# Performance work log

Hardware: AMD Instinct MI355X
Metric: run time of the kernel (lower is better)

## Reference

```python
import jax, jax.numpy as jnp
import numpy as np

GRID = (32, 32)       # SOM grid shape
INPUT_DIM = 512
BATCH = 16384
TAU = 0.5             # softmax temperature
EPS = 1e-8


def setup_inputs() -> dict:
    key = jax.random.key(0)
    k1, k2 = jax.random.split(key)
    x = jax.random.normal(k1, (BATCH, INPUT_DIM), dtype=jnp.float32)
    # glorot_uniform for shape (*GRID, INPUT_DIM): fan_in = 32*32, fan_out = 512
    fan_in, fan_out = GRID[0] * GRID[1], INPUT_DIM
    limit = float(np.sqrt(6.0 / (fan_in + fan_out)))
    weights_map = jax.random.uniform(
        k2, (*GRID, INPUT_DIM), dtype=jnp.float32, minval=-limit, maxval=limit
    )
    return {"x": x, "weights_map": weights_map}


def reference(x, weights_map):
    """SoftSOM forward: squared distances -> per-dimension softmax -> soft reconstruction."""
    B, D = x.shape
    gh, gw = GRID
    w_flat = weights_map.reshape(gh * gw, D)  # [N, D]
    d2 = (
        jnp.sum(x * x, axis=-1, keepdims=True)           # [B,1]
        + jnp.sum(w_flat * w_flat, axis=-1)[None, :]     # [1,N]
        - 2.0 * (x @ w_flat.T)                           # [B,N]
    )
    logits = (-d2 / TAU).reshape(B, gh, gw)
    # per-dimension softmax: softmax along each grid axis, combined multiplicatively
    s_rows = jax.nn.softmax(logits, axis=1)   # softmax over grid dim 0
    s_cols = jax.nn.softmax(logits, axis=2)   # softmax over grid dim 1
    a = s_rows * s_cols
    a = a / (jnp.sum(a, axis=(1, 2), keepdims=True) + EPS)  # renormalize over grid
    # soft reconstruction: weighted sum of prototypes
    y = jnp.einsum("bij,ijd->bd", a, weights_map)  # [B, D]
    return y
```

## Files before the change

### kernel.cpp

```cpp
#include <hip/hip_runtime.h>
#include <hip/hip_bf16.h>
#include <stdint.h>

#define B_SZ 16384
#define D_SZ 512
#define N_SZ 1024

using f16x8 = __attribute__((ext_vector_type(8))) _Float16;
using f16x4 = __attribute__((ext_vector_type(4))) _Float16;
using f32x4 = __attribute__((ext_vector_type(4))) float;

typedef unsigned int u32_as1 __attribute__((address_space(1)));
typedef unsigned int u32_as3 __attribute__((address_space(3)));

__device__ __forceinline__ void gload16(const void* g, void* lds_base) {
    __builtin_amdgcn_global_load_lds((const u32_as1*)g, (u32_as3*)lds_base, 16, 0, 0);
}

__device__ __forceinline__ unsigned short f16bits(_Float16 h) {
    return __builtin_bit_cast(unsigned short, h);
}

__global__ __launch_bounds__(256) void prep(
    const float* __restrict__ W, const float* __restrict__ X,
    _Float16* __restrict__ wh, _Float16* __restrict__ wt,
    float* __restrict__ ww, _Float16* __restrict__ xh) {
    const int bid = blockIdx.x;
    const int t = threadIdx.x;
    if (bid < 32) {
        __shared__ unsigned int cells[512 * 17];
        const int n0 = bid * 32;
        const int np = t >> 4;
        const int dc = t & 15;
        const int na = n0 + 2 * np, nb = na + 1;
        const int d0 = dc * 32;
        float va[32], vb[32];
#pragma unroll
        for (int i = 0; i < 8; ++i) {
            *reinterpret_cast<float4*>(&va[i * 4]) =
                *reinterpret_cast<const float4*>(&W[(size_t)na * D_SZ + d0 + i * 4]);
            *reinterpret_cast<float4*>(&vb[i * 4]) =
                *reinterpret_cast<const float4*>(&W[(size_t)nb * D_SZ + d0 + i * 4]);
        }
        float sa = 0.f, sb = 0.f;
#pragma unroll
        for (int i = 0; i < 32; ++i) { sa += va[i] * va[i]; sb += vb[i] * vb[i]; }
        sa += __shfl_xor(sa, 1); sa += __shfl_xor(sa, 2);
        sa += __shfl_xor(sa, 4); sa += __shfl_xor(sa, 8);
        sb += __shfl_xor(sb, 1); sb += __shfl_xor(sb, 2);
        sb += __shfl_xor(sb, 4); sb += __shfl_xor(sb, 8);
        if (dc == 0) { ww[na] = sa; ww[nb] = sb; }
        _Float16 ha[32], hb[32];
#pragma unroll
        for (int i = 0; i < 32; ++i) { ha[i] = (_Float16)va[i]; hb[i] = (_Float16)vb[i]; }
        unsigned int pa[16], pb[16];
#pragma unroll
        for (int j = 0; j < 16; ++j) {
            pa[j] = (unsigned)f16bits(ha[2 * j]) | ((unsigned)f16bits(ha[2 * j + 1]) << 16);
            pb[j] = (unsigned)f16bits(hb[2 * j]) | ((unsigned)f16bits(hb[2 * j + 1]) << 16);
        }
        unsigned int* whU = reinterpret_cast<unsigned int*>(wh);
#pragma unroll
        for (int j = 0; j < 4; ++j) {
            *reinterpret_cast<uint4*>(&whU[((size_t)na * D_SZ + d0) / 2 + j * 4]) =
                make_uint4(pa[j * 4], pa[j * 4 + 1], pa[j * 4 + 2], pa[j * 4 + 3]);
            *reinterpret_cast<uint4*>(&whU[((size_t)nb * D_SZ + d0) / 2 + j * 4]) =
                make_uint4(pb[j * 4], pb[j * 4 + 1], pb[j * 4 + 2], pb[j * 4 + 3]);
        }
#pragma unroll
        for (int k = 0; k < 32; ++k) {
            const int d = d0 + k;
            const unsigned u = (unsigned)f16bits(ha[k]) | ((unsigned)f16bits(hb[k]) << 16);
            cells[d * 17 + (np ^ ((d >> 5) & 15))] = u;
        }
        __syncthreads();
        for (int rr = 0; rr < 2; ++rr) {
            const int d = 2 * t + rr;
            const int px = (d >> 5) & 15;
            unsigned int buf[16];
#pragma unroll
            for (int j = 0; j < 16; ++j) buf[j] = cells[d * 17 + (j ^ px)];
            unsigned int* wtU = reinterpret_cast<unsigned int*>(wt);
#pragma unroll
            for (int j = 0; j < 4; ++j)
                *reinterpret_cast<uint4*>(&wtU[((size_t)d * N_SZ + n0) / 2 + j * 4]) =
                    make_uint4(buf[j * 4], buf[j * 4 + 1], buf[j * 4 + 2], buf[j * 4 + 3]);
        }
    } else {
        const int b2 = bid - 32;
        const int chunk = (b2 & 7) * 512 + (b2 >> 3);
        const size_t idx = ((size_t)chunk * 256 + t) * 8;
        const float4 a = *reinterpret_cast<const float4*>(&X[idx]);
        const float4 b = *reinterpret_cast<const float4*>(&X[idx + 4]);
        f16x8 h = {(_Float16)a.x, (_Float16)a.y, (_Float16)a.z, (_Float16)a.w,
                   (_Float16)b.x, (_Float16)b.y, (_Float16)b.z, (_Float16)b.w};
        *reinterpret_cast<f16x8*>(&xh[idx]) = h;
    }
}

__global__ __launch_bounds__(256, 4) void gemm1(
    const _Float16* __restrict__ xh, const _Float16* __restrict__ wh,
    const float* __restrict__ ww, _Float16* __restrict__ L16) {
    __shared__ _Float16 smem[16384];
    const int tid = threadIdx.x;
    const int wid = tid >> 6, lane = tid & 63;
    const int raw = blockIdx.y * 8 + blockIdx.x;
    const int wsw = (raw & 7) * 128 + (raw >> 3);
    const int bn0 = (wsw & 7) * 128;
    const int bm0 = (wsw >> 3) * 128;
    const int m0 = (wid >> 1) * 64, n0 = (wid & 1) * 64;
    const int rA = lane & 15;
    const int cbr = (lane >> 4) * 16;
    const int rswz = ((rA >> 1) & 3) << 4;

    const int br0 = (wid * 2) * 16 + (lane >> 2);
    const int br1 = (wid * 2 + 1) * 16 + (lane >> 2);
    const int sg0 = ((lane & 3) ^ ((br0 >> 1) & 3)) * 8;
    const int sg1 = ((lane & 3) ^ ((br1 >> 1) & 3)) * 8;
    const int bdst0 = (wid * 2) * 1024;
    const int bdst1 = (wid * 2 + 1) * 1024;
    char* const As_b = (char*)smem;
    char* const Bs_b = (char*)smem + 16384;

    f32x4 acc[4][4];
    for (int mi = 0; mi < 4; ++mi)
        for (int ni = 0; ni < 4; ++ni) acc[mi][ni] = (f32x4){0.f, 0.f, 0.f, 0.f};

    gload16(&xh[(size_t)(bm0 + br0) * D_SZ + sg0], As_b + bdst0);
    gload16(&xh[(size_t)(bm0 + br1) * D_SZ + sg1], As_b + bdst1);
    gload16(&wh[(size_t)(bn0 + br0) * D_SZ + sg0], Bs_b + bdst0);
    gload16(&wh[(size_t)(bn0 + br1) * D_SZ + sg1], Bs_b + bdst1);
    __syncthreads();

    int cur = 0;
    for (int kt = 0; kt < 16; ++kt) {
        const int nxt = cur ^ 1;
        if (kt < 15) {
            const int gk = (kt + 1) * 32;
            gload16(&xh[(size_t)(bm0 + br0) * D_SZ + gk + sg0], As_b + nxt * 8192 + bdst0);
            gload16(&xh[(size_t)(bm0 + br1) * D_SZ + gk + sg1], As_b + nxt * 8192 + bdst1);
            gload16(&wh[(size_t)(bn0 + br0) * D_SZ + gk + sg0], Bs_b + nxt * 8192 + bdst0);
            gload16(&wh[(size_t)(bn0 + br1) * D_SZ + gk + sg1], Bs_b + nxt * 8192 + bdst1);
        }
        f16x8 af[4], bf[4];
        for (int mi = 0; mi < 4; ++mi)
            af[mi] = *reinterpret_cast<const f16x8*>(
                As_b + cur * 8192 + (m0 + mi * 16 + rA) * 64 + (cbr ^ rswz));
        for (int ni = 0; ni < 4; ++ni)
            bf[ni] = *reinterpret_cast<const f16x8*>(
                Bs_b + cur * 8192 + (n0 + ni * 16 + rA) * 64 + (cbr ^ rswz));
        for (int mi = 0; mi < 4; ++mi)
            for (int ni = 0; ni < 4; ++ni)
                acc[mi][ni] = __builtin_amdgcn_mfma_f32_16x16x32_f16(af[mi], bf[ni], acc[mi][ni], 0, 0, 0);
        __syncthreads();
        cur = nxt;
    }

    for (int mi = 0; mi < 4; ++mi)
        for (int ni = 0; ni < 4; ++ni) {
            const int ln = n0 + ni * 16 + rA;
            const float wwn = ww[bn0 + ln];
            const int lm = m0 + mi * 16 + (lane >> 4) * 4;
            const f32x4 a = acc[mi][ni];
            for (int r = 0; r < 4; ++r)
                smem[(lm + r) * 128 + ln] = (_Float16)(4.f * a[r] - 2.f * wwn);
        }
    __syncthreads();
    for (int c = 0; c < 8; ++c) {
        const int idx = c * 2048 + tid * 8;
        const int row = idx >> 7, col = idx & 127;
        const f16x8 v = *reinterpret_cast<const f16x8*>(&smem[idx]);
        *reinterpret_cast<f16x8*>(&L16[(size_t)(bm0 + row) * N_SZ + bn0 + col]) = v;
    }
}

__global__ __launch_bounds__(512) void softsm(_Float16* __restrict__ L16) {
    __shared__ float4 spart[2][4][8];
    __shared__ float mpart[2][4];
    __shared__ float Tp[2][4];
    const int h = threadIdx.x >> 8;
    const int t = threadIdx.x & 255;
    const int w = t >> 6, lane = t & 63;
    const int g8 = t & 7;
    const int bid = blockIdx.x;
    const size_t row = (size_t)(bid & 7) * 2048 + (size_t)(bid >> 3) * 2 + h;
    const f16x4 lv = *reinterpret_cast<const f16x4*>(&L16[row * N_SZ + (size_t)t * 4]);
    const float v0 = (float)lv[0], v1 = (float)lv[1], v2 = (float)lv[2], v3 = (float)lv[3];

    float m = fmaxf(fmaxf(v0, v1), fmaxf(v2, v3));
    for (int o = 32; o; o >>= 1) m = fmaxf(m, __shfl_xor(m, o));
    if (lane == 0) mpart[h][w] = m;
    __syncthreads();
    m = fmaxf(fmaxf(mpart[h][0], mpart[h][1]), fmaxf(mpart[h][2], mpart[h][3]));

    const float u0 = __expf(v0 - m), u1 = __expf(v1 - m);
    const float u2 = __expf(v2 - m), u3 = __expf(v3 - m);
    float rs = (u0 + u1) + (u2 + u3);
    rs += __shfl_xor(rs, 1); rs += __shfl_xor(rs, 2); rs += __shfl_xor(rs, 4);
    float s0 = u0, s1 = u1, s2 = u2, s3 = u3;
    for (int o = 8; o <= 32; o <<= 1) {
        s0 += __shfl_xor(s0, o); s1 += __shfl_xor(s1, o);
        s2 += __shfl_xor(s2, o); s3 += __shfl_xor(s3, o);
    }
    if (lane < 8) spart[h][w][lane] = make_float4(s0, s1, s2, s3);
    __syncthreads();
    {
        const float4 q0 = spart[h][0][g8], q1 = spart[h][1][g8];
        const float4 q2 = spart[h][2][g8], q3 = spart[h][3][g8];
        s0 = (q0.x + q1.x) + (q2.x + q3.x);
        s1 = (q0.y + q1.y) + (q2.y + q3.y);
        s2 = (q0.z + q1.z) + (q2.z + q3.z);
        s3 = (q0.w + q1.w) + (q2.w + q3.w);
    }
    const float irs = __builtin_amdgcn_rcpf(rs);
    const float t0 = u0 * u0 * irs * __builtin_amdgcn_rcpf(s0);
    const float t1 = u1 * u1 * irs * __builtin_amdgcn_rcpf(s1);
    const float t2 = u2 * u2 * irs * __builtin_amdgcn_rcpf(s2);
    const float t3 = u3 * u3 * irs * __builtin_amdgcn_rcpf(s3);
    float sT = (t0 + t1) + (t2 + t3);
    for (int o = 1; o <= 32; o <<= 1) sT += __shfl_xor(sT, o);
    if (lane == 0) Tp[h][w] = sT;
    __syncthreads();
    const float T = (Tp[h][0] + Tp[h][1]) + (Tp[h][2] + Tp[h][3]);
    const float inv = __builtin_amdgcn_rcpf(T + 1e-8f);
    f16x4 o16 = {(_Float16)(t0 * inv), (_Float16)(t1 * inv),
                 (_Float16)(t2 * inv), (_Float16)(t3 * inv)};
    *reinterpret_cast<f16x4*>(&L16[row * N_SZ + (size_t)t * 4]) = o16;
}

__global__ __launch_bounds__(256, 4) void gemm2(
    const _Float16* __restrict__ a16, const _Float16* __restrict__ wt,
    float* __restrict__ Y) {
    __shared__ _Float16 As[2 * 128 * 32];
    __shared__ _Float16 Bs[2 * 128 * 32];
    const int tid = threadIdx.x;
    const int wid = tid >> 6, lane = tid & 63;
    const int raw = blockIdx.y * 4 + blockIdx.x;
    const int wsw = (raw & 7) * 64 + (raw >> 3);
    const int bn0 = (wsw & 3) * 128;
    const int bm0 = (wsw >> 2) * 128;
    const int m0 = (wid >> 1) * 64, n0 = (wid & 1) * 64;
    const int rA = lane & 15;
    const int cbr = (lane >> 4) * 16;
    const int rswz = ((rA >> 1) & 3) << 4;

    const int br0 = (wid * 2) * 16 + (lane >> 2);
    const int br1 = (wid * 2 + 1) * 16 + (lane >> 2);
    const int sg0 = ((lane & 3) ^ ((br0 >> 1) & 3)) * 8;
    const int sg1 = ((lane & 3) ^ ((br1 >> 1) & 3)) * 8;
    const int bdst0 = (wid * 2) * 1024;
    const int bdst1 = (wid * 2 + 1) * 1024;
    char* const As_b = (char*)As;
    char* const Bs_b = (char*)Bs;

    f32x4 acc[4][4];
    for (int mi = 0; mi < 4; ++mi)
        for (int ni = 0; ni < 4; ++ni) acc[mi][ni] = (f32x4){0.f, 0.f, 0.f, 0.f};

    gload16(&a16[(size_t)(bm0 + br0) * N_SZ + sg0], As_b + bdst0);
    gload16(&a16[(size_t)(bm0 + br1) * N_SZ + sg1], As_b + bdst1);
    gload16(&wt[(size_t)(bn0 + br0) * N_SZ + sg0], Bs_b + bdst0);
    gload16(&wt[(size_t)(bn0 + br1) * N_SZ + sg1], Bs_b + bdst1);
    __syncthreads();

    int cur = 0;
    for (int kt = 0; kt < 32; ++kt) {
        const int nxt = cur ^ 1;
        if (kt < 31) {
            const int gk = (kt + 1) * 32;
            gload16(&a16[(size_t)(bm0 + br0) * N_SZ + gk + sg0], As_b + nxt * 8192 + bdst0);
            gload16(&a16[(size_t)(bm0 + br1) * N_SZ + gk + sg1], As_b + nxt * 8192 + bdst1);
            gload16(&wt[(size_t)(bn0 + br0) * N_SZ + gk + sg0], Bs_b + nxt * 8192 + bdst0);
            gload16(&wt[(size_t)(bn0 + br1) * N_SZ + gk + sg1], Bs_b + nxt * 8192 + bdst1);
        }
        f16x8 af[4], bf[4];
        for (int mi = 0; mi < 4; ++mi)
            af[mi] = *reinterpret_cast<const f16x8*>(
                As_b + cur * 8192 + (m0 + mi * 16 + rA) * 64 + (cbr ^ rswz));
        for (int ni = 0; ni < 4; ++ni)
            bf[ni] = *reinterpret_cast<const f16x8*>(
                Bs_b + cur * 8192 + (n0 + ni * 16 + rA) * 64 + (cbr ^ rswz));
        for (int mi = 0; mi < 4; ++mi)
            for (int ni = 0; ni < 4; ++ni)
                acc[mi][ni] = __builtin_amdgcn_mfma_f32_16x16x32_f16(af[mi], bf[ni], acc[mi][ni], 0, 0, 0);
        __syncthreads();
        cur = nxt;
    }
    for (int mi = 0; mi < 4; ++mi)
        for (int ni = 0; ni < 4; ++ni) {
            const int dd = bn0 + n0 + ni * 16 + rA;
            const int bb = bm0 + m0 + mi * 16 + (lane >> 4) * 4;
            const f32x4 a = acc[mi][ni];
            for (int r = 0; r < 4; ++r)
                Y[(size_t)(bb + r) * D_SZ + dd] = a[r];
        }
}

extern "C" void kernel_launch(void* const* d_in, const int* in_sizes, int n_in,
                              void* d_out, int out_size, void* d_ws, size_t ws_size,
                              hipStream_t stream) {
    (void)in_sizes; (void)n_in; (void)out_size; (void)ws_size;
    const float* X = (const float*)d_in[0];
    const float* W = (const float*)d_in[1];
    float* Y = (float*)d_out;
    char* ws = (char*)d_ws;

    _Float16* L16 = (_Float16*)ws;
    _Float16* wh  = (_Float16*)(ws + (size_t)32 * 1024 * 1024);
    _Float16* wt  = (_Float16*)(ws + (size_t)33 * 1024 * 1024);
    float*    ww  = (float*)   (ws + (size_t)34 * 1024 * 1024);
    _Float16* xh  = (_Float16*)(ws + (size_t)34 * 1024 * 1024 + 4096);

    prep<<<32 + 4096, 256, 0, stream>>>(W, X, wh, wt, ww, xh);
    gemm1<<<dim3(N_SZ / 128, B_SZ / 128), 256, 0, stream>>>(xh, wh, ww, L16);
    softsm<<<B_SZ / 2, 512, 0, stream>>>(L16);
    gemm2<<<dim3(D_SZ / 128, B_SZ / 128), 256, 0, stream>>>(L16, wt, Y);
}
```

Before: 99.46 us.

## Fuse distance GEMM, dual softmax and reconstruction GEMM into one kernel

Replaces the three kernels (gemm1, softsm, gemm2) with one fused kernel. Each 512-thread block owns 64 batch rows across all 1024 grid cells. It keeps logits in registers, does the row, column and total softmax reductions through shuffles and LDS, and writes the normalized weights to a swizzled f16 LDS tile. That tile feeds the second GEMM directly. This removes the 32 MB f16 logits buffer and its write, read and rewrite round trips through global memory. In exchange, operands are read straight from global/L2 with no LDS staging or double buffering, and the large LDS footprint allows only one block (8 waves) per CU, which risks exposed load latency.

After: 112.8 us. 13.5% more time.

```diff
diff --git a/kernel.cpp b/kernel.cpp
--- a/kernel.cpp
+++ b/kernel.cpp
@@ -7,15 +7,7 @@
 #define N_SZ 1024
 
 using f16x8 = __attribute__((ext_vector_type(8))) _Float16;
-using f16x4 = __attribute__((ext_vector_type(4))) _Float16;
 using f32x4 = __attribute__((ext_vector_type(4))) float;
-
-typedef unsigned int u32_as1 __attribute__((address_space(1)));
-typedef unsigned int u32_as3 __attribute__((address_space(3)));
-
-__device__ __forceinline__ void gload16(const void* g, void* lds_base) {
-    __builtin_amdgcn_global_load_lds((const u32_as1*)g, (u32_as3*)lds_base, 16, 0, 0);
-}
 
 __device__ __forceinline__ unsigned short f16bits(_Float16 h) {
     return __builtin_bit_cast(unsigned short, h);
@@ -98,201 +90,193 @@
     }
 }
 
-__global__ __launch_bounds__(256, 4) void gemm1(
+__global__ __launch_bounds__(512, 2) void fused(
     const _Float16* __restrict__ xh, const _Float16* __restrict__ wh,
-    const float* __restrict__ ww, _Float16* __restrict__ L16) {
-    __shared__ _Float16 smem[16384];
+    const _Float16* __restrict__ wt, const float* __restrict__ ww,
+    float* __restrict__ Y) {
+    __shared__ __align__(16) char lds[152064];
+    float* csw = (float*)lds;
+    float* rs  = (float*)(lds + 131072);
+    float* Mx  = (float*)(lds + 139264);
+    float* Tw  = (float*)(lds + 141312);
+    float* Mv  = (float*)(lds + 143360);
+    float* Tv  = (float*)(lds + 143616);
+    float* csf = (float*)(lds + 143872);
+
     const int tid = threadIdx.x;
-    const int wid = tid >> 6, lane = tid & 63;
-    const int raw = blockIdx.y * 8 + blockIdx.x;
-    const int wsw = (raw & 7) * 128 + (raw >> 3);
-    const int bn0 = (wsw & 7) * 128;
-    const int bm0 = (wsw >> 3) * 128;
-    const int m0 = (wid >> 1) * 64, n0 = (wid & 1) * 64;
-    const int rA = lane & 15;
-    const int cbr = (lane >> 4) * 16;
-    const int rswz = ((rA >> 1) & 3) << 4;
-
-    const int br0 = (wid * 2) * 16 + (lane >> 2);
-    const int br1 = (wid * 2 + 1) * 16 + (lane >> 2);
-    const int sg0 = ((lane & 3) ^ ((br0 >> 1) & 3)) * 8;
-    const int sg1 = ((lane & 3) ^ ((br1 >> 1) & 3)) * 8;
-    const int bdst0 = (wid * 2) * 1024;
-    const int bdst1 = (wid * 2 + 1) * 1024;
-    char* const As_b = (char*)smem;
-    char* const Bs_b = (char*)smem + 16384;
-
-    f32x4 acc[4][4];
-    for (int mi = 0; mi < 4; ++mi)
-        for (int ni = 0; ni < 4; ++ni) acc[mi][ni] = (f32x4){0.f, 0.f, 0.f, 0.f};
-
-    gload16(&xh[(size_t)(bm0 + br0) * D_SZ + sg0], As_b + bdst0);
-    gload16(&xh[(size_t)(bm0 + br1) * D_SZ + sg1], As_b + bdst1);
-    gload16(&wh[(size_t)(bn0 + br0) * D_SZ + sg0], Bs_b + bdst0);
-    gload16(&wh[(size_t)(bn0 + br1) * D_SZ + sg1], Bs_b + bdst1);
-    __syncthreads();
-
-    int cur = 0;
+    const int w = tid >> 6, l = tid & 63;
+    const int l4 = l >> 4, lm = l & 15;
+    const int raw = blockIdx.x;
+    const int bm0 = ((raw & 7) * 32 + (raw >> 3)) * 64;
+
+    f32x4 acc[4][8];
+#pragma unroll
+    for (int mi = 0; mi < 4; ++mi)
+#pragma unroll
+        for (int ni = 0; ni < 8; ++ni) acc[mi][ni] = (f32x4){0.f, 0.f, 0.f, 0.f};
+
     for (int kt = 0; kt < 16; ++kt) {
-        const int nxt = cur ^ 1;
-        if (kt < 15) {
-            const int gk = (kt + 1) * 32;
-            gload16(&xh[(size_t)(bm0 + br0) * D_SZ + gk + sg0], As_b + nxt * 8192 + bdst0);
-            gload16(&xh[(size_t)(bm0 + br1) * D_SZ + gk + sg1], As_b + nxt * 8192 + bdst1);
-            gload16(&wh[(size_t)(bn0 + br0) * D_SZ + gk + sg0], Bs_b + nxt * 8192 + bdst0);
-            gload16(&wh[(size_t)(bn0 + br1) * D_SZ + gk + sg1], Bs_b + nxt * 8192 + bdst1);
-        }
-        f16x8 af[4], bf[4];
+        const int gk = kt * 32;
+        f16x8 af[4], bf[8];
+#pragma unroll
         for (int mi = 0; mi < 4; ++mi)
             af[mi] = *reinterpret_cast<const f16x8*>(
-                As_b + cur * 8192 + (m0 + mi * 16 + rA) * 64 + (cbr ^ rswz));
-        for (int ni = 0; ni < 4; ++ni)
+                &xh[(size_t)(bm0 + mi * 16 + lm) * D_SZ + gk + l4 * 8]);
+#pragma unroll
+        for (int ni = 0; ni < 8; ++ni)
             bf[ni] = *reinterpret_cast<const f16x8*>(
-                Bs_b + cur * 8192 + (n0 + ni * 16 + rA) * 64 + (cbr ^ rswz));
+                &wh[(size_t)(w * 128 + ni * 16 + lm) * D_SZ + gk + l4 * 8]);
+#pragma unroll
         for (int mi = 0; mi < 4; ++mi)
-            for (int ni = 0; ni < 4; ++ni)
+#pragma unroll
+            for (int ni = 0; ni < 8; ++ni)
                 acc[mi][ni] = __builtin_amdgcn_mfma_f32_16x16x32_f16(af[mi], bf[ni], acc[mi][ni], 0, 0, 0);
-        __syncthreads();
-        cur = nxt;
-    }
-
-    for (int mi = 0; mi < 4; ++mi)
-        for (int ni = 0; ni < 4; ++ni) {
-            const int ln = n0 + ni * 16 + rA;
-            const float wwn = ww[bn0 + ln];
-            const int lm = m0 + mi * 16 + (lane >> 4) * 4;
-            const f32x4 a = acc[mi][ni];
+    }
+    float wwv[8];
+#pragma unroll
+    for (int ni = 0; ni < 8; ++ni) wwv[ni] = ww[w * 128 + ni * 16 + lm];
+#pragma unroll
+    for (int mi = 0; mi < 4; ++mi)
+#pragma unroll
+        for (int ni = 0; ni < 8; ++ni)
+#pragma unroll
             for (int r = 0; r < 4; ++r)
-                smem[(lm + r) * 128 + ln] = (_Float16)(4.f * a[r] - 2.f * wwn);
-        }
-    __syncthreads();
-    for (int c = 0; c < 8; ++c) {
-        const int idx = c * 2048 + tid * 8;
-        const int row = idx >> 7, col = idx & 127;
-        const f16x8 v = *reinterpret_cast<const f16x8*>(&smem[idx]);
-        *reinterpret_cast<f16x8*>(&L16[(size_t)(bm0 + row) * N_SZ + bn0 + col]) = v;
-    }
-}
-
-__global__ __launch_bounds__(512) void softsm(_Float16* __restrict__ L16) {
-    __shared__ float4 spart[2][4][8];
-    __shared__ float mpart[2][4];
-    __shared__ float Tp[2][4];
-    const int h = threadIdx.x >> 8;
-    const int t = threadIdx.x & 255;
-    const int w = t >> 6, lane = t & 63;
-    const int g8 = t & 7;
-    const int bid = blockIdx.x;
-    const size_t row = (size_t)(bid & 7) * 2048 + (size_t)(bid >> 3) * 2 + h;
-    const f16x4 lv = *reinterpret_cast<const f16x4*>(&L16[row * N_SZ + (size_t)t * 4]);
-    const float v0 = (float)lv[0], v1 = (float)lv[1], v2 = (float)lv[2], v3 = (float)lv[3];
-
-    float m = fmaxf(fmaxf(v0, v1), fmaxf(v2, v3));
-    for (int o = 32; o; o >>= 1) m = fmaxf(m, __shfl_xor(m, o));
-    if (lane == 0) mpart[h][w] = m;
-    __syncthreads();
-    m = fmaxf(fmaxf(mpart[h][0], mpart[h][1]), fmaxf(mpart[h][2], mpart[h][3]));
-
-    const float u0 = __expf(v0 - m), u1 = __expf(v1 - m);
-    const float u2 = __expf(v2 - m), u3 = __expf(v3 - m);
-    float rs = (u0 + u1) + (u2 + u3);
-    rs += __shfl_xor(rs, 1); rs += __shfl_xor(rs, 2); rs += __shfl_xor(rs, 4);
-    float s0 = u0, s1 = u1, s2 = u2, s3 = u3;
-    for (int o = 8; o <= 32; o <<= 1) {
-        s0 += __shfl_xor(s0, o); s1 += __shfl_xor(s1, o);
-        s2 += __shfl_xor(s2, o); s3 += __shfl_xor(s3, o);
-    }
-    if (lane < 8) spart[h][w][lane] = make_float4(s0, s1, s2, s3);
-    __syncthreads();
-    {
-        const float4 q0 = spart[h][0][g8], q1 = spart[h][1][g8];
-        const float4 q2 = spart[h][2][g8], q3 = spart[h][3][g8];
-        s0 = (q0.x + q1.x) + (q2.x + q3.x);
-        s1 = (q0.y + q1.y) + (q2.y + q3.y);
-        s2 = (q0.z + q1.z) + (q2.z + q3.z);
-        s3 = (q0.w + q1.w) + (q2.w + q3.w);
-    }
-    const float irs = __builtin_amdgcn_rcpf(rs);
-    const float t0 = u0 * u0 * irs * __builtin_amdgcn_rcpf(s0);
-    const float t1 = u1 * u1 * irs * __builtin_amdgcn_rcpf(s1);
-    const float t2 = u2 * u2 * irs * __builtin_amdgcn_rcpf(s2);
-    const float t3 = u3 * u3 * irs * __builtin_amdgcn_rcpf(s3);
-    float sT = (t0 + t1) + (t2 + t3);
-    for (int o = 1; o <= 32; o <<= 1) sT += __shfl_xor(sT, o);
-    if (lane == 0) Tp[h][w] = sT;
-    __syncthreads();
-    const float T = (Tp[h][0] + Tp[h][1]) + (Tp[h][2] + Tp[h][3]);
-    const float inv = __builtin_amdgcn_rcpf(T + 1e-8f);
-    f16x4 o16 = {(_Float16)(t0 * inv), (_Float16)(t1 * inv),
-                 (_Float16)(t2 * inv), (_Float16)(t3 * inv)};
-    *reinterpret_cast<f16x4*>(&L16[row * N_SZ + (size_t)t * 4]) = o16;
-}
-
-__global__ __launch_bounds__(256, 4) void gemm2(
-    const _Float16* __restrict__ a16, const _Float16* __restrict__ wt,
-    float* __restrict__ Y) {
-    __shared__ _Float16 As[2 * 128 * 32];
-    __shared__ _Float16 Bs[2 * 128 * 32];
-    const int tid = threadIdx.x;
-    const int wid = tid >> 6, lane = tid & 63;
-    const int raw = blockIdx.y * 4 + blockIdx.x;
-    const int wsw = (raw & 7) * 64 + (raw >> 3);
-    const int bn0 = (wsw & 3) * 128;
-    const int bm0 = (wsw >> 2) * 128;
-    const int m0 = (wid >> 1) * 64, n0 = (wid & 1) * 64;
-    const int rA = lane & 15;
-    const int cbr = (lane >> 4) * 16;
-    const int rswz = ((rA >> 1) & 3) << 4;
-
-    const int br0 = (wid * 2) * 16 + (lane >> 2);
-    const int br1 = (wid * 2 + 1) * 16 + (lane >> 2);
-    const int sg0 = ((lane & 3) ^ ((br0 >> 1) & 3)) * 8;
-    const int sg1 = ((lane & 3) ^ ((br1 >> 1) & 3)) * 8;
-    const int bdst0 = (wid * 2) * 1024;
-    const int bdst1 = (wid * 2 + 1) * 1024;
-    char* const As_b = (char*)As;
-    char* const Bs_b = (char*)Bs;
-
-    f32x4 acc[4][4];
-    for (int mi = 0; mi < 4; ++mi)
-        for (int ni = 0; ni < 4; ++ni) acc[mi][ni] = (f32x4){0.f, 0.f, 0.f, 0.f};
-
-    gload16(&a16[(size_t)(bm0 + br0) * N_SZ + sg0], As_b + bdst0);
-    gload16(&a16[(size_t)(bm0 + br1) * N_SZ + sg1], As_b + bdst1);
-    gload16(&wt[(size_t)(bn0 + br0) * N_SZ + sg0], Bs_b + bdst0);
-    gload16(&wt[(size_t)(bn0 + br1) * N_SZ + sg1], Bs_b + bdst1);
-    __syncthreads();
-
-    int cur = 0;
+                acc[mi][ni][r] = 4.f * acc[mi][ni][r] - 2.f * wwv[ni];
+
+#pragma unroll
+    for (int mi = 0; mi < 4; ++mi)
+#pragma unroll
+        for (int r = 0; r < 4; ++r) {
+            float m = acc[mi][0][r];
+#pragma unroll
+            for (int ni = 1; ni < 8; ++ni) m = fmaxf(m, acc[mi][ni][r]);
+            m = fmaxf(m, __shfl_xor(m, 1));
+            m = fmaxf(m, __shfl_xor(m, 2));
+            m = fmaxf(m, __shfl_xor(m, 4));
+            m = fmaxf(m, __shfl_xor(m, 8));
+            if (lm == 0) Mx[(mi * 16 + l4 * 4 + r) * 8 + w] = m;
+        }
+    __syncthreads();
+    if (tid < 64) {
+        float m = Mx[tid * 8];
+#pragma unroll
+        for (int k = 1; k < 8; ++k) m = fmaxf(m, Mx[tid * 8 + k]);
+        Mv[tid] = m;
+    }
+    __syncthreads();
+#pragma unroll
+    for (int mi = 0; mi < 4; ++mi)
+#pragma unroll
+        for (int r = 0; r < 4; ++r) {
+            const int b = mi * 16 + l4 * 4 + r;
+            const float Mb = Mv[b];
+            float u[8];
+#pragma unroll
+            for (int ni = 0; ni < 8; ++ni) {
+                u[ni] = __expf(acc[mi][ni][r] - Mb);
+                acc[mi][ni][r] = u[ni];
+            }
+#pragma unroll
+            for (int ip = 0; ip < 4; ++ip) {
+                float s = u[2 * ip] + u[2 * ip + 1];
+                s += __shfl_xor(s, 1); s += __shfl_xor(s, 2);
+                s += __shfl_xor(s, 4); s += __shfl_xor(s, 8);
+                if (lm == 0) rs[b * 32 + 4 * w + ip] = s;
+            }
+#pragma unroll
+            for (int jp = 0; jp < 2; ++jp) {
+                const float c = (u[jp] + u[2 + jp]) + (u[4 + jp] + u[6 + jp]);
+                csw[(w * 64 + b) * 32 + jp * 16 + lm] = c;
+            }
+        }
+    __syncthreads();
+    for (int c = tid; c < 2048; c += 512) {
+        float s = csw[c];
+#pragma unroll
+        for (int k = 1; k < 8; ++k) s += csw[k * 2048 + c];
+        csf[c] = s;
+    }
+    __syncthreads();
+#pragma unroll
+    for (int mi = 0; mi < 4; ++mi)
+#pragma unroll
+        for (int r = 0; r < 4; ++r) {
+            const int b = mi * 16 + l4 * 4 + r;
+            float rsv[4], csv[2];
+#pragma unroll
+            for (int ip = 0; ip < 4; ++ip) rsv[ip] = __builtin_amdgcn_rcpf(rs[b * 32 + 4 * w + ip]);
+#pragma unroll
+            for (int jp = 0; jp < 2; ++jp) csv[jp] = __builtin_amdgcn_rcpf(csf[b * 32 + jp * 16 + lm]);
+            float tsum = 0.f;
+#pragma unroll
+            for (int ni = 0; ni < 8; ++ni) {
+                const float uu = acc[mi][ni][r];
+                const float t = uu * uu * rsv[ni >> 1] * csv[ni & 1];
+                acc[mi][ni][r] = t;
+                tsum += t;
+            }
+            tsum += __shfl_xor(tsum, 1); tsum += __shfl_xor(tsum, 2);
+            tsum += __shfl_xor(tsum, 4); tsum += __shfl_xor(tsum, 8);
+            if (lm == 0) Tw[b * 8 + w] = tsum;
+        }
+    __syncthreads();
+    if (tid < 64) {
+        float s = Tw[tid * 8];
+#pragma unroll
+        for (int k = 1; k < 8; ++k) s += Tw[tid * 8 + k];
+        Tv[tid] = __builtin_amdgcn_rcpf(s + 1e-8f);
+    }
+    __syncthreads();
+#pragma unroll
+    for (int mi = 0; mi < 4; ++mi)
+#pragma unroll
+        for (int r = 0; r < 4; ++r) {
+            const int b = mi * 16 + l4 * 4 + r;
+            const float Tb = Tv[b];
+#pragma unroll
+            for (int ni = 0; ni < 8; ++ni) {
+                const int n = w * 128 + ni * 16 + lm;
+                const int off = b * 2048 + ((n * 2) ^ ((b & 7) << 4));
+                *reinterpret_cast<_Float16*>(lds + off) = (_Float16)(acc[mi][ni][r] * Tb);
+            }
+        }
+    __syncthreads();
+
+    f32x4 acc2[4][4];
+#pragma unroll
+    for (int mi = 0; mi < 4; ++mi)
+#pragma unroll
+        for (int di = 0; di < 4; ++di) acc2[mi][di] = (f32x4){0.f, 0.f, 0.f, 0.f};
+
     for (int kt = 0; kt < 32; ++kt) {
-        const int nxt = cur ^ 1;
-        if (kt < 31) {
-            const int gk = (kt + 1) * 32;
-            gload16(&a16[(size_t)(bm0 + br0) * N_SZ + gk + sg0], As_b + nxt * 8192 + bdst0);
-            gload16(&a16[(size_t)(bm0 + br1) * N_SZ + gk + sg1], As_b + nxt * 8192 + bdst1);
-            gload16(&wt[(size_t)(bn0 + br0) * N_SZ + gk + sg0], Bs_b + nxt * 8192 + bdst0);
-            gload16(&wt[(size_t)(bn0 + br1) * N_SZ + gk + sg1], Bs_b + nxt * 8192 + bdst1);
-        }
-        f16x8 af[4], bf[4];
+        f16x8 a4[4], b4[4];
+#pragma unroll
+        for (int mi = 0; mi < 4; ++mi) {
+            const int b = mi * 16 + lm;
+            const int off = b * 2048 + ((kt * 64 + l4 * 16) ^ ((b & 7) << 4));
+            a4[mi] = *reinterpret_cast<const f16x8*>(lds + off);
+        }
+#pragma unroll
+        for (int di = 0; di < 4; ++di) {
+            const int d = w * 64 + di * 16 + lm;
+            b4[di] = *reinterpret_cast<const f16x8*>(
+                &wt[(size_t)d * N_SZ + kt * 32 + l4 * 8]);
+        }
+#pragma unroll
         for (int mi = 0; mi < 4; ++mi)
-            af[mi] = *reinterpret_cast<const f16x8*>(
-                As_b + cur * 8192 + (m0 + mi * 16 + rA) * 64 + (cbr ^ rswz));
-        for (int ni = 0; ni < 4; ++ni)
-            bf[ni] = *reinterpret_cast<const f16x8*>(
-                Bs_b + cur * 8192 + (n0 + ni * 16 + rA) * 64 + (cbr ^ rswz));
-        for (int mi = 0; mi < 4; ++mi)
-            for (int ni = 0; ni < 4; ++ni)
-                acc[mi][ni] = __builtin_amdgcn_mfma_f32_16x16x32_f16(af[mi], bf[ni], acc[mi][ni], 0, 0, 0);
-        __syncthreads();
-        cur = nxt;
-    }
-    for (int mi = 0; mi < 4; ++mi)
-        for (int ni = 0; ni < 4; ++ni) {
-            const int dd = bn0 + n0 + ni * 16 + rA;
-            const int bb = bm0 + m0 + mi * 16 + (lane >> 4) * 4;
-            const f32x4 a = acc[mi][ni];
+#pragma unroll
+            for (int di = 0; di < 4; ++di)
+                acc2[mi][di] = __builtin_amdgcn_mfma_f32_16x16x32_f16(a4[mi], b4[di], acc2[mi][di], 0, 0, 0);
+    }
+#pragma unroll
+    for (int mi = 0; mi < 4; ++mi)
+#pragma unroll
+        for (int di = 0; di < 4; ++di) {
+            const int dd = w * 64 + di * 16 + lm;
+            const int bb = bm0 + mi * 16 + l4 * 4;
+#pragma unroll
             for (int r = 0; r < 4; ++r)
-                Y[(size_t)(bb + r) * D_SZ + dd] = a[r];
+                Y[(size_t)(bb + r) * D_SZ + dd] = acc2[mi][di][r];
         }
 }
 
@@ -305,14 +289,11 @@
     float* Y = (float*)d_out;
     char* ws = (char*)d_ws;
 
-    _Float16* L16 = (_Float16*)ws;
-    _Float16* wh  = (_Float16*)(ws + (size_t)32 * 1024 * 1024);
-    _Float16* wt  = (_Float16*)(ws + (size_t)33 * 1024 * 1024);
-    float*    ww  = (float*)   (ws + (size_t)34 * 1024 * 1024);
-    _Float16* xh  = (_Float16*)(ws + (size_t)34 * 1024 * 1024 + 4096);
+    _Float16* wh = (_Float16*)ws;
+    _Float16* wt = (_Float16*)(ws + (size_t)1 * 1024 * 1024);
+    float*    ww = (float*)   (ws + (size_t)2 * 1024 * 1024);
+    _Float16* xh = (_Float16*)(ws + (size_t)2 * 1024 * 1024 + 4096);
 
     prep<<<32 + 4096, 256, 0, stream>>>(W, X, wh, wt, ww, xh);
-    gemm1<<<dim3(N_SZ / 128, B_SZ / 128), 256, 0, stream>>>(xh, wh, ww, L16);
-    softsm<<<B_SZ / 2, 512, 0, stream>>>(L16);
-    gemm2<<<dim3(D_SZ / 128, B_SZ / 128), 256, 0, stream>>>(L16, wt, Y);
-}
+    fused<<<256, 512, 0, stream>>>(xh, wh, wt, ww, Y);
+}
```

## Fuse X fp16 conversion into gemm1 by staging fp32 tiles in LDS

Applied to the files above, without the earlier changes.

Removes the separate pass in prep that converts X to fp16 and writes it to workspace. gemm1 now DMAs fp32 rows of X straight into an XOR-swizzled LDS buffer and converts them to fp16 while building MFMA fragments. This avoids writing and re-reading a 16 MB fp16 copy of X. In exchange gemm1 reads twice as many A bytes per tile, uses 48 KB of LDS with occupancy lowered to 3 blocks, and adds conversion ALU work in the inner loop.

Measured after the change: 105.1 us. 5.7% more time.

```diff
diff --git a/kernel.cpp b/kernel.cpp
--- a/kernel.cpp
+++ b/kernel.cpp
@@ -22,86 +22,73 @@
 }
 
 __global__ __launch_bounds__(256) void prep(
-    const float* __restrict__ W, const float* __restrict__ X,
-    _Float16* __restrict__ wh, _Float16* __restrict__ wt,
-    float* __restrict__ ww, _Float16* __restrict__ xh) {
-    const int bid = blockIdx.x;
+    const float* __restrict__ W, _Float16* __restrict__ wh,
+    _Float16* __restrict__ wt, float* __restrict__ ww) {
+    __shared__ unsigned int cells[512 * 17];
     const int t = threadIdx.x;
-    if (bid < 32) {
-        __shared__ unsigned int cells[512 * 17];
-        const int n0 = bid * 32;
-        const int np = t >> 4;
-        const int dc = t & 15;
-        const int na = n0 + 2 * np, nb = na + 1;
-        const int d0 = dc * 32;
-        float va[32], vb[32];
-#pragma unroll
-        for (int i = 0; i < 8; ++i) {
-            *reinterpret_cast<float4*>(&va[i * 4]) =
-                *reinterpret_cast<const float4*>(&W[(size_t)na * D_SZ + d0 + i * 4]);
-            *reinterpret_cast<float4*>(&vb[i * 4]) =
-                *reinterpret_cast<const float4*>(&W[(size_t)nb * D_SZ + d0 + i * 4]);
-        }
-        float sa = 0.f, sb = 0.f;
-#pragma unroll
-        for (int i = 0; i < 32; ++i) { sa += va[i] * va[i]; sb += vb[i] * vb[i]; }
-        sa += __shfl_xor(sa, 1); sa += __shfl_xor(sa, 2);
-        sa += __shfl_xor(sa, 4); sa += __shfl_xor(sa, 8);
-        sb += __shfl_xor(sb, 1); sb += __shfl_xor(sb, 2);
-        sb += __shfl_xor(sb, 4); sb += __shfl_xor(sb, 8);
-        if (dc == 0) { ww[na] = sa; ww[nb] = sb; }
-        _Float16 ha[32], hb[32];
-#pragma unroll
-        for (int i = 0; i < 32; ++i) { ha[i] = (_Float16)va[i]; hb[i] = (_Float16)vb[i]; }
-        unsigned int pa[16], pb[16];
-#pragma unroll
-        for (int j = 0; j < 16; ++j) {
-            pa[j] = (unsigned)f16bits(ha[2 * j]) | ((unsigned)f16bits(ha[2 * j + 1]) << 16);
-            pb[j] = (unsigned)f16bits(hb[2 * j]) | ((unsigned)f16bits(hb[2 * j + 1]) << 16);
-        }
-        unsigned int* whU = reinterpret_cast<unsigned int*>(wh);
-#pragma unroll
-        for (int j = 0; j < 4; ++j) {
-            *reinterpret_cast<uint4*>(&whU[((size_t)na * D_SZ + d0) / 2 + j * 4]) =
-                make_uint4(pa[j * 4], pa[j * 4 + 1], pa[j * 4 + 2], pa[j * 4 + 3]);
-            *reinterpret_cast<uint4*>(&whU[((size_t)nb * D_SZ + d0) / 2 + j * 4]) =
-                make_uint4(pb[j * 4], pb[j * 4 + 1], pb[j * 4 + 2], pb[j * 4 + 3]);
-        }
-#pragma unroll
-        for (int k = 0; k < 32; ++k) {
-            const int d = d0 + k;
-            const unsigned u = (unsigned)f16bits(ha[k]) | ((unsigned)f16bits(hb[k]) << 16);
-            cells[d * 17 + (np ^ ((d >> 5) & 15))] = u;
-        }
-        __syncthreads();
-        for (int rr = 0; rr < 2; ++rr) {
-            const int d = 2 * t + rr;
-            const int px = (d >> 5) & 15;
-            unsigned int buf[16];
-#pragma unroll
-            for (int j = 0; j < 16; ++j) buf[j] = cells[d * 17 + (j ^ px)];
-            unsigned int* wtU = reinterpret_cast<unsigned int*>(wt);
-#pragma unroll
-            for (int j = 0; j < 4; ++j)
-                *reinterpret_cast<uint4*>(&wtU[((size_t)d * N_SZ + n0) / 2 + j * 4]) =
-                    make_uint4(buf[j * 4], buf[j * 4 + 1], buf[j * 4 + 2], buf[j * 4 + 3]);
-        }
-    } else {
-        const int b2 = bid - 32;
-        const int chunk = (b2 & 7) * 512 + (b2 >> 3);
-        const size_t idx = ((size_t)chunk * 256 + t) * 8;
-        const float4 a = *reinterpret_cast<const float4*>(&X[idx]);
-        const float4 b = *reinterpret_cast<const float4*>(&X[idx + 4]);
-        f16x8 h = {(_Float16)a.x, (_Float16)a.y, (_Float16)a.z, (_Float16)a.w,
-                   (_Float16)b.x, (_Float16)b.y, (_Float16)b.z, (_Float16)b.w};
-        *reinterpret_cast<f16x8*>(&xh[idx]) = h;
-    }
-}
-
-__global__ __launch_bounds__(256, 4) void gemm1(
-    const _Float16* __restrict__ xh, const _Float16* __restrict__ wh,
+    const int n0 = blockIdx.x * 32;
+    const int np = t >> 4;
+    const int dc = t & 15;
+    const int na = n0 + 2 * np, nb = na + 1;
+    const int d0 = dc * 32;
+    float va[32], vb[32];
+#pragma unroll
+    for (int i = 0; i < 8; ++i) {
+        *reinterpret_cast<float4*>(&va[i * 4]) =
+            *reinterpret_cast<const float4*>(&W[(size_t)na * D_SZ + d0 + i * 4]);
+        *reinterpret_cast<float4*>(&vb[i * 4]) =
+            *reinterpret_cast<const float4*>(&W[(size_t)nb * D_SZ + d0 + i * 4]);
+    }
+    float sa = 0.f, sb = 0.f;
+#pragma unroll
+    for (int i = 0; i < 32; ++i) { sa += va[i] * va[i]; sb += vb[i] * vb[i]; }
+    sa += __shfl_xor(sa, 1); sa += __shfl_xor(sa, 2);
+    sa += __shfl_xor(sa, 4); sa += __shfl_xor(sa, 8);
+    sb += __shfl_xor(sb, 1); sb += __shfl_xor(sb, 2);
+    sb += __shfl_xor(sb, 4); sb += __shfl_xor(sb, 8);
+    if (dc == 0) { ww[na] = sa; ww[nb] = sb; }
+    _Float16 ha[32], hb[32];
+#pragma unroll
+    for (int i = 0; i < 32; ++i) { ha[i] = (_Float16)va[i]; hb[i] = (_Float16)vb[i]; }
+    unsigned int pa[16], pb[16];
+#pragma unroll
+    for (int j = 0; j < 16; ++j) {
+        pa[j] = (unsigned)f16bits(ha[2 * j]) | ((unsigned)f16bits(ha[2 * j + 1]) << 16);
+        pb[j] = (unsigned)f16bits(hb[2 * j]) | ((unsigned)f16bits(hb[2 * j + 1]) << 16);
+    }
+    unsigned int* whU = reinterpret_cast<unsigned int*>(wh);
+#pragma unroll
+    for (int j = 0; j < 4; ++j) {
+        *reinterpret_cast<uint4*>(&whU[((size_t)na * D_SZ + d0) / 2 + j * 4]) =
+            make_uint4(pa[j * 4], pa[j * 4 + 1], pa[j * 4 + 2], pa[j * 4 + 3]);
+        *reinterpret_cast<uint4*>(&whU[((size_t)nb * D_SZ + d0) / 2 + j * 4]) =
+            make_uint4(pb[j * 4], pb[j * 4 + 1], pb[j * 4 + 2], pb[j * 4 + 3]);
+    }
+#pragma unroll
+    for (int k = 0; k < 32; ++k) {
+        const int d = d0 + k;
+        const unsigned u = (unsigned)f16bits(ha[k]) | ((unsigned)f16bits(hb[k]) << 16);
+        cells[d * 17 + (np ^ ((d >> 5) & 15))] = u;
+    }
+    __syncthreads();
+    for (int rr = 0; rr < 2; ++rr) {
+        const int d = 2 * t + rr;
+        const int px = (d >> 5) & 15;
+        unsigned int buf[16];
+#pragma unroll
+        for (int j = 0; j < 16; ++j) buf[j] = cells[d * 17 + (j ^ px)];
+        unsigned int* wtU = reinterpret_cast<unsigned int*>(wt);
+#pragma unroll
+        for (int j = 0; j < 4; ++j)
+            *reinterpret_cast<uint4*>(&wtU[((size_t)d * N_SZ + n0) / 2 + j * 4]) =
+                make_uint4(buf[j * 4], buf[j * 4 + 1], buf[j * 4 + 2], buf[j * 4 + 3]);
+    }
+}
+
+__global__ __launch_bounds__(256, 3) void gemm1(
+    const float* __restrict__ X, const _Float16* __restrict__ wh,
     const float* __restrict__ ww, _Float16* __restrict__ L16) {
-    __shared__ _Float16 smem[16384];
+    __shared__ __align__(16) char lds[49152];
     const int tid = threadIdx.x;
     const int wid = tid >> 6, lane = tid & 63;
     const int raw = blockIdx.y * 8 + blockIdx.x;
@@ -110,26 +97,41 @@
     const int bm0 = (wsw >> 3) * 128;
     const int m0 = (wid >> 1) * 64, n0 = (wid & 1) * 64;
     const int rA = lane & 15;
-    const int cbr = (lane >> 4) * 16;
+    const int l4 = lane >> 4;
+    const int cbr = l4 * 16;
     const int rswz = ((rA >> 1) & 3) << 4;
 
+    const int arow = wid * 32 + (lane >> 3);
+    const int ach = ((lane & 7) ^ (lane >> 3)) * 4;
     const int br0 = (wid * 2) * 16 + (lane >> 2);
     const int br1 = (wid * 2 + 1) * 16 + (lane >> 2);
     const int sg0 = ((lane & 3) ^ ((br0 >> 1) & 3)) * 8;
     const int sg1 = ((lane & 3) ^ ((br1 >> 1) & 3)) * 8;
     const int bdst0 = (wid * 2) * 1024;
     const int bdst1 = (wid * 2 + 1) * 1024;
-    char* const As_b = (char*)smem;
-    char* const Bs_b = (char*)smem + 16384;
+    char* const Bs_b = lds + 32768;
 
     f32x4 acc[4][4];
     for (int mi = 0; mi < 4; ++mi)
         for (int ni = 0; ni < 4; ++ni) acc[mi][ni] = (f32x4){0.f, 0.f, 0.f, 0.f};
 
-    gload16(&xh[(size_t)(bm0 + br0) * D_SZ + sg0], As_b + bdst0);
-    gload16(&xh[(size_t)(bm0 + br1) * D_SZ + sg1], As_b + bdst1);
-    gload16(&wh[(size_t)(bn0 + br0) * D_SZ + sg0], Bs_b + bdst0);
-    gload16(&wh[(size_t)(bn0 + br1) * D_SZ + sg1], Bs_b + bdst1);
+#define STAGE_A(buf, gk)                                                      \
+    {                                                                         \
+        _Pragma("unroll")                                                     \
+        for (int s = 0; s < 4; ++s)                                           \
+            gload16(&X[(size_t)(bm0 + arow + s * 8) * D_SZ + (gk) + ach],     \
+                    lds + (buf) * 16384 + wid * 4096 + s * 1024);             \
+    }
+#define STAGE_B(buf, gk)                                                      \
+    {                                                                         \
+        gload16(&wh[(size_t)(bn0 + br0) * D_SZ + (gk) + sg0],                 \
+                Bs_b + (buf) * 8192 + bdst0);                                 \
+        gload16(&wh[(size_t)(bn0 + br1) * D_SZ + (gk) + sg1],                 \
+                Bs_b + (buf) * 8192 + bdst1);                                 \
+    }
+
+    STAGE_A(0, 0)
+    STAGE_B(0, 0)
     __syncthreads();
 
     int cur = 0;
@@ -137,39 +139,51 @@
         const int nxt = cur ^ 1;
         if (kt < 15) {
             const int gk = (kt + 1) * 32;
-            gload16(&xh[(size_t)(bm0 + br0) * D_SZ + gk + sg0], As_b + nxt * 8192 + bdst0);
-            gload16(&xh[(size_t)(bm0 + br1) * D_SZ + gk + sg1], As_b + nxt * 8192 + bdst1);
-            gload16(&wh[(size_t)(bn0 + br0) * D_SZ + gk + sg0], Bs_b + nxt * 8192 + bdst0);
-            gload16(&wh[(size_t)(bn0 + br1) * D_SZ + gk + sg1], Bs_b + nxt * 8192 + bdst1);
+            STAGE_A(nxt, gk)
+            STAGE_B(nxt, gk)
         }
         f16x8 af[4], bf[4];
-        for (int mi = 0; mi < 4; ++mi)
-            af[mi] = *reinterpret_cast<const f16x8*>(
-                As_b + cur * 8192 + (m0 + mi * 16 + rA) * 64 + (cbr ^ rswz));
+#pragma unroll
+        for (int mi = 0; mi < 4; ++mi) {
+            const int r = m0 + mi * 16 + rA;
+            const int kb = l4 * 2;
+            const f32x4 lo = *reinterpret_cast<const f32x4*>(
+                lds + cur * 16384 + r * 128 + (((kb) ^ (r & 7)) << 4));
+            const f32x4 hi = *reinterpret_cast<const f32x4*>(
+                lds + cur * 16384 + r * 128 + (((kb + 1) ^ (r & 7)) << 4));
+            af[mi] = (f16x8){(_Float16)lo[0], (_Float16)lo[1], (_Float16)lo[2], (_Float16)lo[3],
+                             (_Float16)hi[0], (_Float16)hi[1], (_Float16)hi[2], (_Float16)hi[3]};
+        }
+#pragma unroll
         for (int ni = 0; ni < 4; ++ni)
             bf[ni] = *reinterpret_cast<const f16x8*>(
                 Bs_b + cur * 8192 + (n0 + ni * 16 + rA) * 64 + (cbr ^ rswz));
+#pragma unroll
         for (int mi = 0; mi < 4; ++mi)
+#pragma unroll
             for (int ni = 0; ni < 4; ++ni)
                 acc[mi][ni] = __builtin_amdgcn_mfma_f32_16x16x32_f16(af[mi], bf[ni], acc[mi][ni], 0, 0, 0);
         __syncthreads();
         cur = nxt;
     }
-
+#undef STAGE_A
+#undef STAGE_B
+
+    _Float16* ep = (_Float16*)lds;
     for (int mi = 0; mi < 4; ++mi)
         for (int ni = 0; ni < 4; ++ni) {
             const int ln = n0 + ni * 16 + rA;
             const float wwn = ww[bn0 + ln];
-            const int lm = m0 + mi * 16 + (lane >> 4) * 4;
+            const int lm = m0 + mi * 16 + l4 * 4;
             const f32x4 a = acc[mi][ni];
             for (int r = 0; r < 4; ++r)
-                smem[(lm + r) * 128 + ln] = (_Float16)(4.f * a[r] - 2.f * wwn);
+                ep[(lm + r) * 128 + ln] = (_Float16)(4.f * a[r] - 2.f * wwn);
         }
     __syncthreads();
     for (int c = 0; c < 8; ++c) {
         const int idx = c * 2048 + tid * 8;
         const int row = idx >> 7, col = idx & 127;
-        const f16x8 v = *reinterpret_cast<const f16x8*>(&smem[idx]);
+        const f16x8 v = *reinterpret_cast<const f16x8*>(&ep[idx]);
         *reinterpret_cast<f16x8*>(&L16[(size_t)(bm0 + row) * N_SZ + bn0 + col]) = v;
     }
 }
@@ -309,10 +323,9 @@
     _Float16* wh  = (_Float16*)(ws + (size_t)32 * 1024 * 1024);
     _Float16* wt  = (_Float16*)(ws + (size_t)33 * 1024 * 1024);
     float*    ww  = (float*)   (ws + (size_t)34 * 1024 * 1024);
-    _Float16* xh  = (_Float16*)(ws + (size_t)34 * 1024 * 1024 + 4096);
-
-    prep<<<32 + 4096, 256, 0, stream>>>(W, X, wh, wt, ww, xh);
-    gemm1<<<dim3(N_SZ / 128, B_SZ / 128), 256, 0, stream>>>(xh, wh, ww, L16);
+
+    prep<<<32, 256, 0, stream>>>(W, wh, wt, ww);
+    gemm1<<<dim3(N_SZ / 128, B_SZ / 128), 256, 0, stream>>>(X, wh, ww, L16);
     softsm<<<B_SZ / 2, 512, 0, stream>>>(L16);
     gemm2<<<dim3(D_SZ / 128, B_SZ / 128), 256, 0, stream>>>(L16, wt, Y);
 }
```
